# Kernel tuning notes

Measured on AMD Instinct MI355X. Metric: run time of the kernel, lower is better.

## Reference

```python
import jax, jax.numpy as jnp
import numpy as np

B, N, F_DIM, OUT_DIM = 8, 2048, 128, 128

def setup_inputs() -> dict:
    key = jax.random.key(0)
    k1, k2, k3, k4, k5 = jax.random.split(key, 5)
    return {
        "x": jax.random.normal(k1, (B, N, F_DIM), dtype=jnp.float32),
        "adj_w": jax.random.normal(k2, (2 * F_DIM,), dtype=jnp.float32) * (1.0 / np.sqrt(2 * F_DIM)),
        "adj_b": jax.random.normal(k3, (), dtype=jnp.float32),
        "weight": jax.random.normal(k4, (F_DIM, OUT_DIM), dtype=jnp.float32) * (1.0 / np.sqrt(F_DIM)),
        "bias": jax.random.normal(k5, (OUT_DIM,), dtype=jnp.float32),
    }

def reference(x, adj_w, adj_b, weight, bias):
    # x: [B, N, F]. adj[b,i,j] = Linear(concat(x_i, x_j)) = x_i@w1 + x_j@w2 + b
    Bb, Nn, Ff = x.shape
    a_i = x @ adj_w[:Ff]           # [B, N]
    a_j = x @ adj_w[Ff:]           # [B, N]
    adj = a_i[:, :, None] + a_j[:, None, :] + adj_b   # [B, N, N]
    adj = adj + jnp.eye(Nn, dtype=adj.dtype)          # adj[:, i, i] += 1
    out = x @ weight                                  # [B, N, out]
    deg_inv_sqrt = jnp.maximum(adj.sum(axis=-1), 1.0) ** -0.5  # clamp(min=1).pow(-0.5)
    adj = deg_inv_sqrt[:, :, None] * adj * deg_inv_sqrt[:, None, :]
    out = jnp.matmul(adj, out) + bias
    return jax.nn.relu(out)
```

## Files before the change

### kernel.cpp

```cpp
#include <hip/hip_runtime.h>

#define N_ 2048
#define F_ 128

#define WS_P1 0
#define WS_SF 512
#define WS_P2 2560

typedef __attribute__((ext_vector_type(8))) short short8v;
typedef __attribute__((ext_vector_type(4))) float f32x4;
typedef unsigned long long u64;

__device__ inline short f2bf(float f) {
    union { float f; unsigned u; } c; c.f = f;
    unsigned r = (c.u + 0x7FFFu + ((c.u >> 16) & 1u)) >> 16;
    return (short)r;
}
__device__ inline void store_pair(u64* p, float f) {
    union { float f; unsigned u; } c; c.f = f;
    const u64 v = ((u64)(~c.u) << 32) | (u64)c.u;
    __hip_atomic_store(p, v, __ATOMIC_RELAXED, __HIP_MEMORY_SCOPE_AGENT);
}
__device__ inline bool pair_ok(u64 v) {
    return (unsigned)(v >> 32) == (unsigned)(~(unsigned)v);
}
__device__ inline float pair_val(u64 v) {
    union { unsigned u; float f; } c; c.u = (unsigned)v;
    return c.f;
}

__global__ __launch_bounds__(256, 2) void gcn_one(
    const float* __restrict__ x, const float* __restrict__ adj_w,
    const float* __restrict__ adj_b_p, const float* __restrict__ weight,
    const float* __restrict__ bias, float* __restrict__ outx,
    u64* __restrict__ P1, u64* __restrict__ SF, u64* __restrict__ P2)
{
    __shared__ unsigned short wt[128 * 128];
    __shared__ float adjw[256];
    __shared__ float ail[32], ajl[32];
    __shared__ float disl[32], ajdl[32];
    __shared__ float red0[4][64], red1[4][64];
    __shared__ float s0l[128], s1l[128], bl[128];
    __shared__ float Ash;

    const int bid = blockIdx.x;
    const int b = bid >> 6, kbme = bid & 63, r0 = kbme * 32;
    const int t = threadIdx.x;
    const int lane = t & 63, w = t >> 6;
    const int u = lane & 15, g = lane >> 4;

    adjw[t] = adj_w[t];
    if (t < 128) bl[t] = bias[t];
    __syncthreads();

    {
        const int row = t >> 3, kseg = t & 7;
        const float* xp = x + (size_t)(b * N_ + r0 + row) * F_ + kseg * 16;
        float ai = 0.f, aj = 0.f;
        #pragma unroll
        for (int p = 0; p < 4; ++p) {
            const float4 v = *reinterpret_cast<const float4*>(xp + p * 4);
            const float vv[4] = {v.x, v.y, v.z, v.w};
            #pragma unroll
            for (int q = 0; q < 4; ++q) {
                const int k = kseg * 16 + p * 4 + q;
                ai = fmaf(vv[q], adjw[k], ai);
                aj = fmaf(vv[q], adjw[128 + k], aj);
            }
        }
        #pragma unroll
        for (int m = 1; m < 8; m <<= 1) {
            ai += __shfl_xor(ai, m, 64);
            aj += __shfl_xor(aj, m, 64);
        }
        if (kseg == 0) { ail[row] = ai + adj_b_p[0]; ajl[row] = aj; }
    }
    __syncthreads();
    if (t < 32) {
        float s = ajl[t];
        #pragma unroll
        for (int off = 16; off > 0; off >>= 1) s += __shfl_down(s, off, 64);
        if (t == 0) store_pair(&P1[bid], s);
    }

    {
        const int c = t & 127, khalf = t >> 7;
        for (int j8 = 0; j8 < 8; ++j8) {
            const int kb = khalf * 8 + j8;
            short8v v;
            #pragma unroll
            for (int i = 0; i < 8; ++i)
                v[i] = f2bf(weight[(kb * 8 + i) * F_ + c]);
            const int slot = kb ^ (c & 15);
            *reinterpret_cast<short8v*>(&wt[c * 128 + slot * 8]) = v;
        }
    }
    __syncthreads();

    const int wr = (w & 1) * 16;
    const int ct0 = (w >> 1) * 4;
    f32x4 acc[4];
    #pragma unroll
    for (int i = 0; i < 4; ++i) acc[i] = (f32x4)(0.f);
    {
        const float* xrow = x + (size_t)(b * N_ + r0 + wr + u) * F_;
        #pragma unroll
        for (int kk = 0; kk < 4; ++kk) {
            const float4 xa = *reinterpret_cast<const float4*>(xrow + kk * 32 + g * 8);
            const float4 xb = *reinterpret_cast<const float4*>(xrow + kk * 32 + g * 8 + 4);
            short8v af;
            af[0] = f2bf(xa.x); af[1] = f2bf(xa.y); af[2] = f2bf(xa.z); af[3] = f2bf(xa.w);
            af[4] = f2bf(xb.x); af[5] = f2bf(xb.y); af[6] = f2bf(xb.z); af[7] = f2bf(xb.w);
            const int kb = kk * 4 + g;
            #pragma unroll
            for (int c = 0; c < 4; ++c) {
                const int col = (ct0 + c) * 16 + u;
                const int slot = kb ^ u;
                const short8v bfv = *reinterpret_cast<const short8v*>(&wt[col * 128 + slot * 8]);
                acc[c] = __builtin_amdgcn_mfma_f32_16x16x32_bf16(af, bfv, acc[c], 0, 0, 0);
            }
        }
    }

    if (t < 64) {
        u64 v;
        while (true) {
            v = __hip_atomic_load(&P1[b * 64 + t], __ATOMIC_RELAXED, __HIP_MEMORY_SCOPE_AGENT);
            if (pair_ok(v)) break;
            __builtin_amdgcn_s_sleep(2);
        }
        float s = pair_val(v);
        #pragma unroll
        for (int off = 32; off > 0; off >>= 1) s += __shfl_down(s, off, 64);
        if (t == 0) Ash = s;
    }
    __syncthreads();
    if (t < 32) {
        const float deg = fmaxf(2048.f * ail[t] + Ash + 1.f, 1.f);
        const float d = rsqrtf(deg);
        disl[t] = d;
        ajdl[t] = ajl[t] * d;
    }
    __syncthreads();

    {
        float p0[4], p1[4];
        #pragma unroll
        for (int c = 0; c < 4; ++c) {
            float s0 = 0.f, s1 = 0.f;
            #pragma unroll
            for (int r = 0; r < 4; ++r) {
                const int row = wr + g * 4 + r;
                s0 = fmaf(disl[row], acc[c][r], s0);
                s1 = fmaf(ajdl[row], acc[c][r], s1);
            }
            s0 += __shfl_xor(s0, 16, 64); s0 += __shfl_xor(s0, 32, 64);
            s1 += __shfl_xor(s1, 16, 64); s1 += __shfl_xor(s1, 32, 64);
            p0[c] = s0; p1[c] = s1;
        }
        if (g == 0) {
            #pragma unroll
            for (int c = 0; c < 4; ++c) {
                red0[w][c * 16 + u] = p0[c];
                red1[w][c * 16 + u] = p1[c];
            }
        }
    }
    __syncthreads();
    {
        const int c = t & 127, vec = t >> 7;
        const int cg = c >> 6, cc = c & 63;
        const float v = (vec == 0)
            ? (red0[2 * cg][cc] + red0[2 * cg + 1][cc])
            : (red1[2 * cg][cc] + red1[2 * cg + 1][cc]);
        store_pair(&P2[((size_t)((b * 128 + c) * 2 + vec) << 6) + kbme], v);
    }

    if (kbme < 4) {
        const int p = t >> 2, klo = (t & 3) * 16;
        const int c = kbme * 32 + (p >> 1), vec = p & 1;
        u64* base = &P2[(size_t)((b * 128 + c) * 2 + vec) << 6];
        u64 vv[16];
        bool ok;
        do {
            ok = true;
            #pragma unroll
            for (int i = 0; i < 16; ++i)
                vv[i] = __hip_atomic_load(&base[klo + i], __ATOMIC_RELAXED, __HIP_MEMORY_SCOPE_AGENT);
            #pragma unroll
            for (int i = 0; i < 16; ++i) ok &= pair_ok(vv[i]);
            if (!ok) __builtin_amdgcn_s_sleep(4);
        } while (!ok);
        float s = 0.f;
        #pragma unroll
        for (int i = 0; i < 16; ++i) s += pair_val(vv[i]);
        s += __shfl_xor(s, 1, 64);
        s += __shfl_xor(s, 2, 64);
        if ((t & 3) == 0)
            store_pair(&SF[(b * 128 + c) * 2 + vec], s);
    }

    {
        const int c = t & 127, vec = t >> 7;
        u64 v;
        while (true) {
            v = __hip_atomic_load(&SF[(b * 128 + c) * 2 + vec], __ATOMIC_RELAXED, __HIP_MEMORY_SCOPE_AGENT);
            if (pair_ok(v)) break;
            __builtin_amdgcn_s_sleep(2);
        }
        if (vec == 0) s0l[c] = pair_val(v); else s1l[c] = pair_val(v);
    }
    __syncthreads();

    #pragma unroll
    for (int c = 0; c < 4; ++c) {
        const int col = (ct0 + c) * 16 + u;
        const float sv0 = s0l[col], sv1 = s1l[col], bv = bl[col];
        #pragma unroll
        for (int r = 0; r < 4; ++r) {
            const int row = wr + g * 4 + r;
            const float d = disl[row], ab = ail[row];
            const float o = fmaxf(d * (ab * sv0 + sv1 + d * acc[c][r]) + bv, 0.f);
            outx[(size_t)(b * N_ + r0 + row) * F_ + col] = o;
        }
    }
}

extern "C" void kernel_launch(void* const* d_in, const int* in_sizes, int n_in,
                              void* d_out, int out_size, void* d_ws, size_t ws_size,
                              hipStream_t stream) {
    const float* x      = (const float*)d_in[0];
    const float* adj_w  = (const float*)d_in[1];
    const float* adj_b  = (const float*)d_in[2];
    const float* weight = (const float*)d_in[3];
    const float* bias   = (const float*)d_in[4];
    float* out = (float*)d_out;
    u64* ws = (u64*)d_ws;

    gcn_one<<<512, 256, 0, stream>>>(x, adj_w, adj_b, weight, bias, out,
                                     ws + WS_P1, ws + WS_SF, ws + WS_P2);
}
```

Before: 22.26 us.

## Use 64-row blocks and drop the second-level cross-block reduction stage

Doubles rows per block (256 blocks of 512 threads instead of 512 of 256), so each batch has 32 blocks. Every block now reduces all 32 P2 partials for its batch itself, removing the SF stage and the extra grid-wide wait on the designated reducer blocks. The x row loads are reused for both the adjacency dot products and the MFMA operands, which avoids a second global read. The trade is redundant reads of the partials by every block and fewer, larger blocks, which may reduce occupancy.

```diff
diff --git a/kernel.cpp b/kernel.cpp
--- a/kernel.cpp
+++ b/kernel.cpp
@@ -4,8 +4,7 @@
 #define F_ 128
 
 #define WS_P1 0
-#define WS_SF 512
-#define WS_P2 2560
+#define WS_P2 256
 
 typedef __attribute__((ext_vector_type(8))) short short8v;
 typedef __attribute__((ext_vector_type(4))) float f32x4;
@@ -29,64 +28,74 @@
     return c.f;
 }
 
-__global__ __launch_bounds__(256, 2) void gcn_one(
+__global__ __launch_bounds__(512, 1) void gcn_one(
     const float* __restrict__ x, const float* __restrict__ adj_w,
     const float* __restrict__ adj_b_p, const float* __restrict__ weight,
     const float* __restrict__ bias, float* __restrict__ outx,
-    u64* __restrict__ P1, u64* __restrict__ SF, u64* __restrict__ P2)
+    u64* __restrict__ P1, u64* __restrict__ P2)
 {
     __shared__ unsigned short wt[128 * 128];
     __shared__ float adjw[256];
-    __shared__ float ail[32], ajl[32];
-    __shared__ float disl[32], ajdl[32];
-    __shared__ float red0[4][64], red1[4][64];
+    __shared__ float ail[64], ajl[64], disl[64], ajdl[64];
+    __shared__ float red0[4][128], red1[4][128];
     __shared__ float s0l[128], s1l[128], bl[128];
     __shared__ float Ash;
 
     const int bid = blockIdx.x;
-    const int b = bid >> 6, kbme = bid & 63, r0 = kbme * 32;
+    const int b = bid >> 5, kbme = bid & 31, r0 = kbme * 64;
     const int t = threadIdx.x;
     const int lane = t & 63, w = t >> 6;
     const int u = lane & 15, g = lane >> 4;
-
-    adjw[t] = adj_w[t];
+    const int wr = (w & 3) * 16;
+    const int ct0 = (w >> 2) * 4;
+
+    if (t < 256) adjw[t] = adj_w[t];
     if (t < 128) bl[t] = bias[t];
     __syncthreads();
 
+    const float* xrow = x + (size_t)(b * N_ + r0 + wr + u) * F_;
+    float4 xa[4], xb[4];
+    #pragma unroll
+    for (int kk = 0; kk < 4; ++kk) {
+        xa[kk] = *reinterpret_cast<const float4*>(xrow + kk * 32 + g * 8);
+        xb[kk] = *reinterpret_cast<const float4*>(xrow + kk * 32 + g * 8 + 4);
+    }
     {
-        const int row = t >> 3, kseg = t & 7;
-        const float* xp = x + (size_t)(b * N_ + r0 + row) * F_ + kseg * 16;
         float ai = 0.f, aj = 0.f;
         #pragma unroll
-        for (int p = 0; p < 4; ++p) {
-            const float4 v = *reinterpret_cast<const float4*>(xp + p * 4);
-            const float vv[4] = {v.x, v.y, v.z, v.w};
+        for (int kk = 0; kk < 4; ++kk) {
+            const float va[4] = {xa[kk].x, xa[kk].y, xa[kk].z, xa[kk].w};
+            const float vb[4] = {xb[kk].x, xb[kk].y, xb[kk].z, xb[kk].w};
             #pragma unroll
-            for (int q = 0; q < 4; ++q) {
-                const int k = kseg * 16 + p * 4 + q;
-                ai = fmaf(vv[q], adjw[k], ai);
-                aj = fmaf(vv[q], adjw[128 + k], aj);
+            for (int i = 0; i < 4; ++i) {
+                const int k = kk * 32 + g * 8 + i;
+                ai = fmaf(va[i], adjw[k], ai);
+                aj = fmaf(va[i], adjw[128 + k], aj);
+                ai = fmaf(vb[i], adjw[k + 4], ai);
+                aj = fmaf(vb[i], adjw[128 + k + 4], aj);
             }
         }
-        #pragma unroll
-        for (int m = 1; m < 8; m <<= 1) {
-            ai += __shfl_xor(ai, m, 64);
-            aj += __shfl_xor(aj, m, 64);
-        }
-        if (kseg == 0) { ail[row] = ai + adj_b_p[0]; ajl[row] = aj; }
-    }
-    __syncthreads();
-    if (t < 32) {
+        ai += __shfl_xor(ai, 16, 64); ai += __shfl_xor(ai, 32, 64);
+        aj += __shfl_xor(aj, 16, 64); aj += __shfl_xor(aj, 32, 64);
+        if (w < 4 && g == 0) {
+            ail[wr + u] = ai + adj_b_p[0];
+            ajl[wr + u] = aj;
+        }
+    }
+    __syncthreads();
+
+    if (t < 64) {
         float s = ajl[t];
         #pragma unroll
-        for (int off = 16; off > 0; off >>= 1) s += __shfl_down(s, off, 64);
-        if (t == 0) store_pair(&P1[bid], s);
+        for (int off = 32; off > 0; off >>= 1) s += __shfl_down(s, off, 64);
+        if (t == 0) store_pair(&P1[b * 32 + kbme], s);
     }
 
     {
-        const int c = t & 127, khalf = t >> 7;
-        for (int j8 = 0; j8 < 8; ++j8) {
-            const int kb = khalf * 8 + j8;
+        const int c = t & 127, q = t >> 7;
+        #pragma unroll
+        for (int j = 0; j < 4; ++j) {
+            const int kb = q * 4 + j;
             short8v v;
             #pragma unroll
             for (int i = 0; i < 8; ++i)
@@ -97,45 +106,40 @@
     }
     __syncthreads();
 
-    const int wr = (w & 1) * 16;
-    const int ct0 = (w >> 1) * 4;
     f32x4 acc[4];
     #pragma unroll
     for (int i = 0; i < 4; ++i) acc[i] = (f32x4)(0.f);
-    {
-        const float* xrow = x + (size_t)(b * N_ + r0 + wr + u) * F_;
-        #pragma unroll
-        for (int kk = 0; kk < 4; ++kk) {
-            const float4 xa = *reinterpret_cast<const float4*>(xrow + kk * 32 + g * 8);
-            const float4 xb = *reinterpret_cast<const float4*>(xrow + kk * 32 + g * 8 + 4);
-            short8v af;
-            af[0] = f2bf(xa.x); af[1] = f2bf(xa.y); af[2] = f2bf(xa.z); af[3] = f2bf(xa.w);
-            af[4] = f2bf(xb.x); af[5] = f2bf(xb.y); af[6] = f2bf(xb.z); af[7] = f2bf(xb.w);
-            const int kb = kk * 4 + g;
-            #pragma unroll
-            for (int c = 0; c < 4; ++c) {
-                const int col = (ct0 + c) * 16 + u;
-                const int slot = kb ^ u;
-                const short8v bfv = *reinterpret_cast<const short8v*>(&wt[col * 128 + slot * 8]);
-                acc[c] = __builtin_amdgcn_mfma_f32_16x16x32_bf16(af, bfv, acc[c], 0, 0, 0);
-            }
-        }
-    }
-
-    if (t < 64) {
+    #pragma unroll
+    for (int kk = 0; kk < 4; ++kk) {
+        short8v af;
+        af[0] = f2bf(xa[kk].x); af[1] = f2bf(xa[kk].y);
+        af[2] = f2bf(xa[kk].z); af[3] = f2bf(xa[kk].w);
+        af[4] = f2bf(xb[kk].x); af[5] = f2bf(xb[kk].y);
+        af[6] = f2bf(xb[kk].z); af[7] = f2bf(xb[kk].w);
+        const int kb = kk * 4 + g;
+        #pragma unroll
+        for (int c = 0; c < 4; ++c) {
+            const int col = (ct0 + c) * 16 + u;
+            const int slot = kb ^ u;
+            const short8v bfv = *reinterpret_cast<const short8v*>(&wt[col * 128 + slot * 8]);
+            acc[c] = __builtin_amdgcn_mfma_f32_16x16x32_bf16(af, bfv, acc[c], 0, 0, 0);
+        }
+    }
+
+    if (t < 32) {
         u64 v;
         while (true) {
-            v = __hip_atomic_load(&P1[b * 64 + t], __ATOMIC_RELAXED, __HIP_MEMORY_SCOPE_AGENT);
+            v = __hip_atomic_load(&P1[b * 32 + t], __ATOMIC_RELAXED, __HIP_MEMORY_SCOPE_AGENT);
             if (pair_ok(v)) break;
-            __builtin_amdgcn_s_sleep(2);
+            __builtin_amdgcn_s_sleep(1);
         }
         float s = pair_val(v);
         #pragma unroll
-        for (int off = 32; off > 0; off >>= 1) s += __shfl_down(s, off, 64);
+        for (int off = 16; off > 0; off >>= 1) s += __shfl_down(s, off, 32);
         if (t == 0) Ash = s;
     }
     __syncthreads();
-    if (t < 32) {
+    if (t < 64) {
         const float deg = fmaxf(2048.f * ail[t] + Ash + 1.f, 1.f);
         const float d = rsqrtf(deg);
         disl[t] = d;
@@ -143,72 +147,51 @@
     }
     __syncthreads();
 
-    {
-        float p0[4], p1[4];
-        #pragma unroll
-        for (int c = 0; c < 4; ++c) {
-            float s0 = 0.f, s1 = 0.f;
+    #pragma unroll
+    for (int c = 0; c < 4; ++c) {
+        float s0 = 0.f, s1 = 0.f;
+        #pragma unroll
+        for (int r = 0; r < 4; ++r) {
+            const int row = wr + g * 4 + r;
+            s0 = fmaf(disl[row], acc[c][r], s0);
+            s1 = fmaf(ajdl[row], acc[c][r], s1);
+        }
+        s0 += __shfl_xor(s0, 16, 64); s0 += __shfl_xor(s0, 32, 64);
+        s1 += __shfl_xor(s1, 16, 64); s1 += __shfl_xor(s1, 32, 64);
+        if (g == 0) {
+            red0[w & 3][(ct0 + c) * 16 + u] = s0;
+            red1[w & 3][(ct0 + c) * 16 + u] = s1;
+        }
+    }
+    __syncthreads();
+    if (t < 256) {
+        const int c = t & 127;
+        const float v = (t < 128)
+            ? (red0[0][c] + red0[1][c] + red0[2][c] + red0[3][c])
+            : (red1[0][c] + red1[1][c] + red1[2][c] + red1[3][c]);
+        store_pair(&P2[(size_t)(b * 256 + t) * 32 + kbme], v);
+    }
+
+    if (t < 256) {
+        u64* base = &P2[(size_t)(b * 256 + t) * 32];
+        float s = 0.f;
+        #pragma unroll
+        for (int half = 0; half < 2; ++half) {
+            u64 vv[16];
+            bool ok;
+            do {
+                ok = true;
+                #pragma unroll
+                for (int i = 0; i < 16; ++i)
+                    vv[i] = __hip_atomic_load(&base[half * 16 + i], __ATOMIC_RELAXED, __HIP_MEMORY_SCOPE_AGENT);
+                #pragma unroll
+                for (int i = 0; i < 16; ++i) ok &= pair_ok(vv[i]);
+                if (!ok) __builtin_amdgcn_s_sleep(2);
+            } while (!ok);
             #pragma unroll
-            for (int r = 0; r < 4; ++r) {
-                const int row = wr + g * 4 + r;
-                s0 = fmaf(disl[row], acc[c][r], s0);
-                s1 = fmaf(ajdl[row], acc[c][r], s1);
-            }
-            s0 += __shfl_xor(s0, 16, 64); s0 += __shfl_xor(s0, 32, 64);
-            s1 += __shfl_xor(s1, 16, 64); s1 += __shfl_xor(s1, 32, 64);
-            p0[c] = s0; p1[c] = s1;
-        }
-        if (g == 0) {
-            #pragma unroll
-            for (int c = 0; c < 4; ++c) {
-                red0[w][c * 16 + u] = p0[c];
-                red1[w][c * 16 + u] = p1[c];
-            }
-        }
-    }
-    __syncthreads();
-    {
-        const int c = t & 127, vec = t >> 7;
-        const int cg = c >> 6, cc = c & 63;
-        const float v = (vec == 0)
-            ? (red0[2 * cg][cc] + red0[2 * cg + 1][cc])
-            : (red1[2 * cg][cc] + red1[2 * cg + 1][cc]);
-        store_pair(&P2[((size_t)((b * 128 + c) * 2 + vec) << 6) + kbme], v);
-    }
-
-    if (kbme < 4) {
-        const int p = t >> 2, klo = (t & 3) * 16;
-        const int c = kbme * 32 + (p >> 1), vec = p & 1;
-        u64* base = &P2[(size_t)((b * 128 + c) * 2 + vec) << 6];
-        u64 vv[16];
-        bool ok;
-        do {
-            ok = true;
-            #pragma unroll
-            for (int i = 0; i < 16; ++i)
-                vv[i] = __hip_atomic_load(&base[klo + i], __ATOMIC_RELAXED, __HIP_MEMORY_SCOPE_AGENT);
-            #pragma unroll
-            for (int i = 0; i < 16; ++i) ok &= pair_ok(vv[i]);
-            if (!ok) __builtin_amdgcn_s_sleep(4);
-        } while (!ok);
-        float s = 0.f;
-        #pragma unroll
-        for (int i = 0; i < 16; ++i) s += pair_val(vv[i]);
-        s += __shfl_xor(s, 1, 64);
-        s += __shfl_xor(s, 2, 64);
-        if ((t & 3) == 0)
-            store_pair(&SF[(b * 128 + c) * 2 + vec], s);
-    }
-
-    {
-        const int c = t & 127, vec = t >> 7;
-        u64 v;
-        while (true) {
-            v = __hip_atomic_load(&SF[(b * 128 + c) * 2 + vec], __ATOMIC_RELAXED, __HIP_MEMORY_SCOPE_AGENT);
-            if (pair_ok(v)) break;
-            __builtin_amdgcn_s_sleep(2);
-        }
-        if (vec == 0) s0l[c] = pair_val(v); else s1l[c] = pair_val(v);
+            for (int i = 0; i < 16; ++i) s += pair_val(vv[i]);
+        }
+        if (t < 128) s0l[t] = s; else s1l[t - 128] = s;
     }
     __syncthreads();
 
@@ -237,6 +220,6 @@
     float* out = (float*)d_out;
     u64* ws = (u64*)d_ws;
 
-    gcn_one<<<512, 256, 0, stream>>>(x, adj_w, adj_b, weight, bias, out,
-                                     ws + WS_P1, ws + WS_SF, ws + WS_P2);
-}
+    gcn_one<<<256, 512, 0, stream>>>(x, adj_w, adj_b, weight, bias, out,
+                                     ws + WS_P1, ws + WS_P2);
+}
```

Measured after the change: 26.75 us. 20.2% more time.
